# Performance work log

Hardware: AMD Instinct MI355X
Metric: run time of the kernel (lower is better)

The kernel has to match this reference:

```python
import jax, jax.numpy as jnp
import numpy as np

B, S, D, H = 4, 2048, 1024, 16
DK = D // H

def setup_inputs() -> dict:
    key = jax.random.key(0)
    ks = jax.random.split(key, 8)
    query = jax.random.normal(ks[0], (B, S, D), dtype=jnp.float32)
    k_in = jax.random.normal(ks[1], (B, S, D), dtype=jnp.float32)
    v_in = jax.random.normal(ks[2], (B, S, D), dtype=jnp.float32)
    # causal mask: 1 where attending allowed, 0 masked (module masks where mask==0)
    mask = jnp.broadcast_to(jnp.tril(jnp.ones((S, S), dtype=jnp.int32)), (B, S, S))
    s = 1.0 / np.sqrt(D)
    w_q = jax.random.normal(ks[3], (D, D), dtype=jnp.float32) * s
    w_k = jax.random.normal(ks[4], (D, D), dtype=jnp.float32) * s
    w_v = jax.random.normal(ks[5], (D, D), dtype=jnp.float32) * s
    w_o = jax.random.normal(ks[6], (D, D), dtype=jnp.float32) * s
    b_o = jnp.zeros((D,), dtype=jnp.float32)
    return {"query": query, "key": k_in, "value": v_in, "mask": mask,
            "w_q": w_q, "w_k": w_k, "w_v": w_v, "w_o": w_o, "b_o": b_o}

def reference(query, key, value, mask, w_q, w_k, w_v, w_o, b_o):
    b, s, d = query.shape
    # projections (nn.Linear: x @ W.T); weights stored as [out, in]
    Q = (query @ w_q.T).reshape(b, s, H, DK).transpose(0, 2, 1, 3)  # [b,h,s,dk]
    K = (key   @ w_k.T).reshape(b, s, H, DK).transpose(0, 2, 1, 3)
    V = (value @ w_v.T).reshape(b, s, H, DK).transpose(0, 2, 1, 3)
    scores = jnp.einsum('bhqd,bhkd->bhqk', Q, K) / np.sqrt(DK)  # [b,h,s,s]
    m = mask[:, None, :, :]  # broadcast over heads
    scores = jnp.where(m == 0, jnp.float32(-1e9), scores)
    attn = jax.nn.softmax(scores, axis=-1)
    out = jnp.einsum('bhqk,bhkd->bhqd', attn, V)  # [b,h,s,dk]
    out = out.transpose(0, 2, 1, 3).reshape(b, s, d)
    out = out @ w_o.T + b_o
    return (out, attn)
```

## Files before the change

### kernel.cpp

```cpp
#include <hip/hip_runtime.h>
#include <hip/hip_bf16.h>

typedef __attribute__((ext_vector_type(8))) short bf16x8;
typedef __attribute__((ext_vector_type(4))) float f32x4;

constexpr int Bn = 4, Sn = 2048, Dn = 1024, Hn = 16;
constexpr int Mn = Bn * Sn;
constexpr float C_SCALE = 0.18033688f;

static __device__ __forceinline__ unsigned short f2bf(float f) {
  union { float f; unsigned int u; } v; v.f = f;
  unsigned int r = v.u + 0x7fffu + ((v.u >> 16) & 1u);
  return (unsigned short)(r >> 16);
}

static __device__ __forceinline__ unsigned int cvtpk_bf16(float lo, float hi) {
  unsigned int r;
  asm("v_cvt_pk_bf16_f32 %0, %1, %2" : "=v"(r) : "v"(lo), "v"(hi));
  return r;
}

static __device__ __forceinline__ void gload_lds16(const unsigned short* g,
                                                   unsigned short* l) {
  __builtin_amdgcn_global_load_lds(
      (const __attribute__((address_space(1))) unsigned int*)g,
      (__attribute__((address_space(3))) unsigned int*)l,
      16, 0, 0);
}

__global__ __launch_bounds__(256)
void cvt7(const float* __restrict__ q, const float* __restrict__ k,
          const float* __restrict__ v, const float* __restrict__ wq,
          const float* __restrict__ wk, const float* __restrict__ wv,
          const float* __restrict__ wo,
          unsigned short* __restrict__ oq, unsigned short* __restrict__ ok,
          unsigned short* __restrict__ ov, unsigned short* __restrict__ owq,
          unsigned short* __restrict__ owk, unsigned short* __restrict__ owv,
          unsigned short* __restrict__ owo)
{
  constexpr size_t NX = (size_t)Mn * Dn;
  constexpr size_t NW = (size_t)Dn * Dn;
  constexpr size_t total = 3 * NX + 4 * NW;
  size_t e = ((size_t)blockIdx.x * blockDim.x + threadIdx.x) * 4;
  const size_t step = (size_t)gridDim.x * blockDim.x * 4;
  for (; e < total; e += step) {
    int seg; size_t off;
    if (e < 3 * NX) { seg = (int)(e >> 23); off = e & (NX - 1); }
    else { const size_t j = e - 3 * NX; seg = 3 + (int)(j >> 20); off = j & (NW - 1); }
    const float* src; unsigned short* dst;
    switch (seg) {
      case 0: src = q;  dst = oq;  break;
      case 1: src = k;  dst = ok;  break;
      case 2: src = v;  dst = ov;  break;
      case 3: src = wq; dst = owq; break;
      case 4: src = wk; dst = owk; break;
      case 5: src = wv; dst = owv; break;
      default: src = wo; dst = owo; break;
    }
    const float4 val = *(const float4*)(src + off);
    ushort4 o;
    o.x = f2bf(val.x); o.y = f2bf(val.y); o.z = f2bf(val.z); o.w = f2bf(val.w);
    *(ushort4*)(dst + off) = o;
  }
}

static __device__ __forceinline__ void gemm_core(
    const unsigned short* __restrict__ A, const unsigned short* __restrict__ Bw,
    unsigned short* Asl, unsigned short* Bsl,
    int m0, int n0, int wave, int lane, f32x4 (*acc)[4])
{
  const int tid = wave * 64 + lane;
  const int lr = lane & 15, lg = lane >> 4;
  const int wm = wave >> 1, wn = wave & 1;

  for (int k0 = 0; k0 < 1024; k0 += 64) {
    __syncthreads();
    #pragma unroll
    for (int it = 0; it < 4; ++it) {
      const int e = it * 256 + tid;
      const int row = e >> 3;
      const int col = ((e & 7) ^ (row & 7)) * 8;
      gload_lds16(A  + (size_t)(m0 + row) * 1024 + k0 + col,
                  &Asl[(it * 256 + wave * 64) * 8]);
      gload_lds16(Bw + (size_t)(n0 + row) * 1024 + k0 + col,
                  &Bsl[(it * 256 + wave * 64) * 8]);
    }
    __syncthreads();

    #pragma unroll
    for (int kk = 0; kk < 2; ++kk) {
      const int ch = ((kk * 4 + lg) ^ (lr & 7)) * 8;
      bf16x8 af[4], bfr[4];
      #pragma unroll
      for (int mf = 0; mf < 4; ++mf)
        af[mf] = *(const bf16x8*)&Asl[(wm * 64 + mf * 16 + lr) * 64 + ch];
      #pragma unroll
      for (int nf = 0; nf < 4; ++nf)
        bfr[nf] = *(const bf16x8*)&Bsl[(wn * 64 + nf * 16 + lr) * 64 + ch];
      #pragma unroll
      for (int mf = 0; mf < 4; ++mf)
        #pragma unroll
        for (int nf = 0; nf < 4; ++nf)
          acc[mf][nf] = __builtin_amdgcn_mfma_f32_16x16x32_bf16(
              af[mf], bfr[nf], acc[mf][nf], 0, 0, 0);
    }
  }
}

__global__ __launch_bounds__(256)
void gemm_qkv(const unsigned short* __restrict__ Xq,
              const unsigned short* __restrict__ Xk,
              const unsigned short* __restrict__ Xv,
              const unsigned short* __restrict__ Wq,
              const unsigned short* __restrict__ Wk,
              const unsigned short* __restrict__ Wv,
              unsigned short* __restrict__ Qbf,
              unsigned short* __restrict__ Kbf,
              unsigned short* __restrict__ Vtb)
{
  __shared__ unsigned short ShBuf[128 * 136];
  unsigned short* Asl = ShBuf;
  unsigned short* Bsl = ShBuf + 128 * 64;

  const int tid  = threadIdx.x;
  const int wave = tid >> 6, lane = tid & 63;
  const int lr = lane & 15, lg = lane >> 4;
  const int wm = wave >> 1, wn = wave & 1;
  const int m0 = blockIdx.x * 128;
  const int n0 = blockIdx.y * 128;
  const int z  = blockIdx.z;

  const unsigned short* A  = (z == 0) ? Xq : (z == 1) ? Xk : Xv;
  const unsigned short* Bw = (z == 0) ? Wq : (z == 1) ? Wk : Wv;

  f32x4 acc[4][4] = {};
  gemm_core(A, Bw, Asl, Bsl, m0, n0, wave, lane, acc);

  if (z < 2) {
    unsigned short* C = (z == 0) ? Qbf : Kbf;
    const float cs = (z == 0) ? C_SCALE : 1.0f;
    #pragma unroll
    for (int mf = 0; mf < 4; ++mf)
      #pragma unroll
      for (int nf = 0; nf < 4; ++nf)
        #pragma unroll
        for (int i = 0; i < 4; ++i) {
          const int row = m0 + wm * 64 + mf * 16 + lg * 4 + i;
          const int col = n0 + wn * 64 + nf * 16 + lr;
          C[(size_t)row * 1024 + col] = f2bf(acc[mf][nf][i] * cs);
        }
  } else {
    unsigned short (*Ts)[136] = (unsigned short (*)[136])ShBuf;
    __syncthreads();
    #pragma unroll
    for (int mf = 0; mf < 4; ++mf)
      #pragma unroll
      for (int nf = 0; nf < 4; ++nf)
        #pragma unroll
        for (int i = 0; i < 4; ++i)
          Ts[wn * 64 + nf * 16 + lr][wm * 64 + mf * 16 + lg * 4 + i] =
              f2bf(acc[mf][nf][i]);
    __syncthreads();
    const int dkl = tid >> 1;
    const int sh  = (tid & 1) * 64;
    const int b = m0 >> 11, s0 = m0 & 2047;
    const int gcol = n0 + dkl;
    const int h = gcol >> 6, dk = gcol & 63;
    unsigned short* dst =
        Vtb + ((size_t)((b * 16 + h) * 64 + dk)) * Sn + s0 + sh;
    #pragma unroll
    for (int jj = 0; jj < 8; ++jj)
      *(bf16x8*)(dst + jj * 8) = *(const bf16x8*)&Ts[dkl][sh + jj * 8];
  }
}

__global__ __launch_bounds__(256)
void gemm_o(const unsigned short* __restrict__ A,
            const unsigned short* __restrict__ Bw,
            float* __restrict__ C, const float* __restrict__ bias)
{
  __shared__ unsigned short Asl[128 * 64];
  __shared__ unsigned short Bsl[128 * 64];
  const int tid  = threadIdx.x;
  const int wave = tid >> 6, lane = tid & 63;
  const int lr = lane & 15, lg = lane >> 4;
  const int wm = wave >> 1, wn = wave & 1;
  const int m0 = blockIdx.x * 128;
  const int n0 = blockIdx.y * 128;

  f32x4 acc[4][4] = {};
  gemm_core(A, Bw, Asl, Bsl, m0, n0, wave, lane, acc);

  float bv[4];
  #pragma unroll
  for (int nf = 0; nf < 4; ++nf) bv[nf] = bias[n0 + wn * 64 + nf * 16 + lr];
  #pragma unroll
  for (int mf = 0; mf < 4; ++mf)
    #pragma unroll
    for (int nf = 0; nf < 4; ++nf)
      #pragma unroll
      for (int i = 0; i < 4; ++i) {
        const int row = m0 + wm * 64 + mf * 16 + lg * 4 + i;
        const int col = n0 + wn * 64 + nf * 16 + lr;
        C[(size_t)row * 1024 + col] = acc[mf][nf][i] + bv[nf];
      }
}

__global__ __launch_bounds__(128)
void attn_fused(const unsigned short* __restrict__ Qb,
                const unsigned short* __restrict__ Kb,
                const unsigned short* __restrict__ Vt,
                float* __restrict__ attn_out,
                unsigned short* __restrict__ Ob)
{
  __shared__ unsigned short Ps[2][32][88];

  const int tid = threadIdx.x;
  const int w = tid >> 6, lane = tid & 63;
  const int lr = lane & 15, lg = lane >> 4;
  const int wg = (blockIdx.x & 7) * 256 + (blockIdx.x >> 3);
  const int bh = wg >> 5;
  const int j  = wg & 31;
  const int qs = w ? (63 - j) : j;
  const int b = bh >> 4, h = bh & 15;
  const int q0 = qs * 32;
  const int nkt = (q0 + 31) / 64 + 1;
  const int kl  = nkt - 1;

  const unsigned short* Kbh = Kb + (size_t)(b * Sn) * Dn + h * 64;
  const unsigned short* Vbh = Vt + (size_t)(bh * 64) * Sn;
  float* aout = attn_out + (size_t)bh * Sn * (size_t)Sn;

  bf16x8 qf[2][2];
  #pragma unroll
  for (int hf = 0; hf < 2; ++hf) {
    const int qoff = (b * Sn + q0 + hf * 16 + lr) * Dn + h * 64 + lg * 8;
    qf[hf][0] = *(const bf16x8*)(Qb + qoff);
    qf[hf][1] = *(const bf16x8*)(Qb + qoff + 32);
  }

  float l[2] = {0.f, 0.f};

  for (int kt = 0; kt < kl; ++kt) {
    bf16x8 kf[4][2];
    #pragma unroll
    for (int nf = 0; nf < 4; ++nf)
      #pragma unroll
      for (int kk = 0; kk < 2; ++kk)
        kf[nf][kk] = *(const bf16x8*)(
            Kbh + (kt * 64 + nf * 16 + lr) * Dn + kk * 32 + lg * 8);
    __builtin_amdgcn_s_setprio(1);
    #pragma unroll
    for (int hf = 0; hf < 2; ++hf)
      #pragma unroll
      for (int nf = 0; nf < 4; ++nf) {
        f32x4 a = {0.f, 0.f, 0.f, 0.f};
        a = __builtin_amdgcn_mfma_f32_16x16x32_bf16(kf[nf][0], qf[hf][0], a, 0, 0, 0);
        a = __builtin_amdgcn_mfma_f32_16x16x32_bf16(kf[nf][1], qf[hf][1], a, 0, 0, 0);
        l[hf] += (exp2f(a[0]) + exp2f(a[1])) + (exp2f(a[2]) + exp2f(a[3]));
      }
    __builtin_amdgcn_s_setprio(0);
  }
  {
    bf16x8 kf[4][2];
    #pragma unroll
    for (int nf = 0; nf < 4; ++nf)
      #pragma unroll
      for (int kk = 0; kk < 2; ++kk)
        kf[nf][kk] = *(const bf16x8*)(
            Kbh + (kl * 64 + nf * 16 + lr) * Dn + kk * 32 + lg * 8);
    #pragma unroll
    for (int hf = 0; hf < 2; ++hf) {
      const int q = q0 + hf * 16 + lr;
      #pragma unroll
      for (int nf = 0; nf < 4; ++nf) {
        f32x4 a = {0.f, 0.f, 0.f, 0.f};
        a = __builtin_amdgcn_mfma_f32_16x16x32_bf16(kf[nf][0], qf[hf][0], a, 0, 0, 0);
        a = __builtin_amdgcn_mfma_f32_16x16x32_bf16(kf[nf][1], qf[hf][1], a, 0, 0, 0);
        #pragma unroll
        for (int i = 0; i < 4; ++i) {
          const int key = kl * 64 + nf * 16 + lg * 4 + i;
          l[hf] += (key <= q) ? exp2f(a[i]) : 0.f;
        }
      }
    }
  }
  float nlg[2];
  #pragma unroll
  for (int hf = 0; hf < 2; ++hf) {
    l[hf] += __shfl_xor(l[hf], 16, 64);
    l[hf] += __shfl_xor(l[hf], 32, 64);
    nlg[hf] = -log2f(l[hf]);
  }

  f32x4 oacc[2][4] = {};
  for (int kt = 0; kt < nkt; ++kt) {
    const bool last = (kt == kl);
    bf16x8 kf[4][2], vt[4][2];
    #pragma unroll
    for (int nf = 0; nf < 4; ++nf)
      #pragma unroll
      for (int kk = 0; kk < 2; ++kk) {
        kf[nf][kk] = *(const bf16x8*)(
            Kbh + (kt * 64 + nf * 16 + lr) * Dn + kk * 32 + lg * 8);
        vt[nf][kk] = *(const bf16x8*)(
            Vbh + (nf * 16 + lr) * Sn + kt * 64 + kk * 32 + lg * 8);
      }
    #pragma unroll
    for (int hf = 0; hf < 2; ++hf) {
      const int q = q0 + hf * 16 + lr;
      __builtin_amdgcn_s_setprio(1);
      #pragma unroll
      for (int nf = 0; nf < 4; ++nf) {
        f32x4 a = {0.f, 0.f, 0.f, 0.f};
        a = __builtin_amdgcn_mfma_f32_16x16x32_bf16(kf[nf][0], qf[hf][0], a, 0, 0, 0);
        a = __builtin_amdgcn_mfma_f32_16x16x32_bf16(kf[nf][1], qf[hf][1], a, 0, 0, 0);
        f32x4 p4;
        if (!last) {
          #pragma unroll
          for (int i = 0; i < 4; ++i) p4[i] = exp2f(a[i] + nlg[hf]);
        } else {
          #pragma unroll
          for (int i = 0; i < 4; ++i) {
            const int key = kl * 64 + nf * 16 + lg * 4 + i;
            const float v = exp2f(a[i] + nlg[hf]);
            p4[i] = (key <= q) ? v : 0.f;
          }
        }
        __builtin_nontemporal_store(
            p4, (f32x4*)&aout[q * Sn + kt * 64 + nf * 16 + lg * 4]);
        uint2 pk;
        pk.x = cvtpk_bf16(p4[0], p4[1]);
        pk.y = cvtpk_bf16(p4[2], p4[3]);
        *(uint2*)&Ps[w][hf * 16 + lr][nf * 16 + lg * 4] = pk;
      }
      __builtin_amdgcn_s_setprio(0);
    }
    __builtin_amdgcn_s_setprio(1);
    #pragma unroll
    for (int hf = 0; hf < 2; ++hf) {
      bf16x8 pa[2];
      pa[0] = *(const bf16x8*)&Ps[w][hf * 16 + lr][lg * 8];
      pa[1] = *(const bf16x8*)&Ps[w][hf * 16 + lr][32 + lg * 8];
      #pragma unroll
      for (int kk = 0; kk < 2; ++kk)
        #pragma unroll
        for (int nf = 0; nf < 4; ++nf)
          oacc[hf][nf] = __builtin_amdgcn_mfma_f32_16x16x32_bf16(
              pa[kk], vt[nf][kk], oacc[hf][nf], 0, 0, 0);
    }
    __builtin_amdgcn_s_setprio(0);
  }
  for (int kt = nkt; kt < Sn / 64; ++kt) {
    const f32x4 z = {0.f, 0.f, 0.f, 0.f};
    #pragma unroll
    for (int jj = 0; jj < 8; ++jj) {
      const int r = q0 + lg + 4 * jj;
      __builtin_nontemporal_store(
          z, (f32x4*)&aout[r * Sn + kt * 64 + lr * 4]);
    }
  }
  #pragma unroll
  for (int hf = 0; hf < 2; ++hf)
    #pragma unroll
    for (int nf = 0; nf < 4; ++nf)
      #pragma unroll
      for (int i = 0; i < 4; ++i) {
        const int qq = q0 + hf * 16 + lg * 4 + i;
        const int dk = nf * 16 + lr;
        Ob[(b * Sn + qq) * Dn + h * 64 + dk] = f2bf(oacc[hf][nf][i]);
      }
}

extern "C" void kernel_launch(void* const* d_in, const int* in_sizes, int n_in,
                              void* d_out, int out_size, void* d_ws, size_t ws_size,
                              hipStream_t stream)
{
  const float* query = (const float*)d_in[0];
  const float* key   = (const float*)d_in[1];
  const float* value = (const float*)d_in[2];
  const float* w_q = (const float*)d_in[4];
  const float* w_k = (const float*)d_in[5];
  const float* w_v = (const float*)d_in[6];
  const float* w_o = (const float*)d_in[7];
  const float* b_o = (const float*)d_in[8];

  constexpr size_t NX = (size_t)Mn * Dn;
  constexpr size_t NW = (size_t)Dn * Dn;
  unsigned short* Xq  = (unsigned short*)d_ws;
  unsigned short* Xk  = Xq  + NX;
  unsigned short* Xv  = Xk  + NX;
  unsigned short* Wq  = Xv  + NX;
  unsigned short* Wk  = Wq  + NW;
  unsigned short* Wv  = Wk  + NW;
  unsigned short* Wo  = Wv  + NW;
  unsigned short* Qbf = Wo  + NW;
  unsigned short* Kbf = Qbf + NX;
  unsigned short* Vtb = Kbf + NX;
  unsigned short* Obf = Vtb + NX;

  float* out  = (float*)d_out;
  float* attn = out + NX;

  cvt7<<<dim3(2048), dim3(256), 0, stream>>>(query, key, value, w_q, w_k, w_v, w_o,
                                             Xq, Xk, Xv, Wq, Wk, Wv, Wo);
  gemm_qkv<<<dim3(Mn / 128, Dn / 128, 3), dim3(256), 0, stream>>>(
      Xq, Xk, Xv, Wq, Wk, Wv, Qbf, Kbf, Vtb);
  attn_fused<<<dim3(64 * 32), dim3(128), 0, stream>>>(Qbf, Kbf, Vtb, attn, Obf);
  gemm_o<<<dim3(Mn / 128, Dn / 128), dim3(256), 0, stream>>>(Obf, Wo, out, b_o);
}
```

Baseline: 451.9 us.

## Add 256x256 double-buffered 8-wave GEMM for Q/K and output projections

```diff
diff --git a/kernel.cpp b/kernel.cpp
--- a/kernel.cpp
+++ b/kernel.cpp
@@ -64,6 +64,151 @@
   }
 }
 
+#define BARm()  asm volatile("s_barrier" ::: "memory")
+#define LGKM0() do { asm volatile("s_waitcnt lgkmcnt(0)" ::: "memory"); \
+                     __builtin_amdgcn_sched_barrier(0); } while (0)
+#define VM4()   asm volatile("s_waitcnt vmcnt(4)" ::: "memory")
+#define VM0()   asm volatile("s_waitcnt vmcnt(0)" ::: "memory")
+
+static __device__ __forceinline__ bf16x8 ldfrag(const unsigned short* half,
+                                                int row, int colB) {
+  int qb = row * 128 + colB;
+  qb ^= (row & 7) << 4;
+  return *(const bf16x8*)((const char*)half + qb);
+}
+
+#define LA_(d, h) (L + (d) * 32768 + (h) * 8192)
+#define LB_(d, h) (L + (d) * 32768 + 16384 + (h) * 8192)
+#define MYA(d)    (L + (d) * 32768 + wm * 8192)
+#define MYB(d)    (L + (d) * 32768 + 16384 + (wn >> 1) * 8192)
+
+#define STAGE_A(d, h, t) do { \
+  const unsigned short* g_ = Ag + (size_t)(m0 + (h) * 128) * 1024 + (t) * 64; \
+  gload_lds16(g_ + (size_t)sr0 * 1024 + sc0, LA_(d, h) + wid * 512); \
+  gload_lds16(g_ + (size_t)sr1 * 1024 + sc1, LA_(d, h) + 4096 + wid * 512); \
+} while (0)
+
+#define STAGE_B(d, h, t) do { \
+  const unsigned short* g_ = Wg + (size_t)(n0 + (h) * 128) * 1024 + (t) * 64; \
+  gload_lds16(g_ + (size_t)sr0 * 1024 + sc0, LB_(d, h) + wid * 512); \
+  gload_lds16(g_ + (size_t)sr1 * 1024 + sc1, LB_(d, h) + 4096 + wid * 512); \
+} while (0)
+
+#define LDQ0(d) do { \
+  _Pragma("unroll") for (int j = 0; j < 4; ++j) { \
+    Ar[j][0] = ldfrag(MYA(d), j * 16 + lr, lg * 16); \
+    Ar[j][1] = ldfrag(MYA(d), j * 16 + lr, 64 + lg * 16); } \
+  _Pragma("unroll") for (int n = 0; n < 2; ++n) { \
+    Br[n][0] = ldfrag(MYB(d), brow + n * 16 + lr, lg * 16); \
+    Br[n][1] = ldfrag(MYB(d), brow + n * 16 + lr, 64 + lg * 16); } \
+} while (0)
+
+#define LDB23(d) do { \
+  _Pragma("unroll") for (int n = 2; n < 4; ++n) { \
+    Br[n][0] = ldfrag(MYB(d), brow + n * 16 + lr, lg * 16); \
+    Br[n][1] = ldfrag(MYB(d), brow + n * 16 + lr, 64 + lg * 16); } \
+} while (0)
+
+#define LDA47(d) do { \
+  _Pragma("unroll") for (int j = 0; j < 4; ++j) { \
+    Ar[j][0] = ldfrag(MYA(d), 64 + j * 16 + lr, lg * 16); \
+    Ar[j][1] = ldfrag(MYA(d), 64 + j * 16 + lr, 64 + lg * 16); } \
+} while (0)
+
+#define QUAD(mb, nb) do { \
+  __builtin_amdgcn_s_setprio(1); \
+  _Pragma("unroll") for (int j = 0; j < 4; ++j) \
+    _Pragma("unroll") for (int n = 0; n < 2; ++n) \
+      _Pragma("unroll") for (int kk2 = 0; kk2 < 2; ++kk2) \
+        acc[(mb) + j][(nb) + n] = __builtin_amdgcn_mfma_f32_16x16x32_bf16( \
+            Ar[j][kk2], Br[(nb) + n][kk2], acc[(mb) + j][(nb) + n], 0, 0, 0); \
+  __builtin_amdgcn_s_setprio(0); \
+  __builtin_amdgcn_sched_barrier(0); \
+} while (0)
+
+template<int OUT>
+__global__ __launch_bounds__(512)
+void gemm256(const unsigned short* __restrict__ A0,
+             const unsigned short* __restrict__ A1,
+             const unsigned short* __restrict__ W0,
+             const unsigned short* __restrict__ W1,
+             unsigned short* __restrict__ C0,
+             unsigned short* __restrict__ C1,
+             float* __restrict__ Cf, const float* __restrict__ bias)
+{
+  __shared__ __align__(16) unsigned short L[65536];
+  const int tid = threadIdx.x;
+  const int wid = tid >> 6, lane = tid & 63;
+  const int lr = lane & 15, lg = lane >> 4;
+  const int wm = wid >> 2, wn = wid & 3;
+  const int m0 = blockIdx.x * 256;
+  const int n0 = blockIdx.y * 256;
+  const int z  = blockIdx.z;
+  const unsigned short* Ag = z ? A1 : A0;
+  const unsigned short* Wg = z ? W1 : W0;
+  const int brow = (wn & 1) * 64;
+
+  const int sr0 = tid >> 3,          sc0 = ((tid & 7) ^ (sr0 & 7)) * 8;
+  const int sr1 = 64 + (tid >> 3),   sc1 = ((tid & 7) ^ (sr1 & 7)) * 8;
+
+  f32x4 acc[8][4] = {};
+  bf16x8 Ar[4][2], Br[4][2];
+
+  STAGE_A(0, 0, 0); STAGE_A(0, 1, 0);
+  STAGE_B(0, 0, 0); STAGE_B(0, 1, 0);
+  STAGE_B(1, 0, 1); STAGE_B(1, 1, 1);
+  VM4(); BARm();
+
+  for (int i = 0; i < 7; ++i) {
+    const int t1 = 2 * i + 1, t2 = t1 + 1, t3 = t1 + 2;
+    LDQ0(0);  STAGE_A(1, 0, t1); BARm(); LGKM0(); QUAD(0, 0); BARm();
+    LDB23(0); STAGE_A(1, 1, t1); BARm(); LGKM0(); QUAD(0, 2); BARm();
+    LDA47(0); STAGE_B(0, 0, t2); BARm(); LGKM0(); QUAD(4, 2); BARm();
+    STAGE_B(0, 1, t2);           BARm();          QUAD(4, 0); VM4(); BARm();
+    LDQ0(1);  STAGE_A(0, 0, t2); BARm(); LGKM0(); QUAD(0, 0); BARm();
+    LDB23(1); STAGE_A(0, 1, t2); BARm(); LGKM0(); QUAD(0, 2); BARm();
+    LDA47(1); STAGE_B(1, 0, t3); BARm(); LGKM0(); QUAD(4, 2); BARm();
+    STAGE_B(1, 1, t3);           BARm();          QUAD(4, 0); VM4(); BARm();
+  }
+  LDQ0(0);  STAGE_A(1, 0, 15); BARm(); LGKM0(); QUAD(0, 0); BARm();
+  LDB23(0); STAGE_A(1, 1, 15); BARm(); LGKM0(); QUAD(0, 2); BARm();
+  LDA47(0);                    BARm(); LGKM0(); QUAD(4, 2); BARm();
+                               BARm();          QUAD(4, 0); VM0(); BARm();
+  LDQ0(1);                     BARm(); LGKM0(); QUAD(0, 0); BARm();
+  LDB23(1);                    BARm(); LGKM0(); QUAD(0, 2); BARm();
+  LDA47(1);                    BARm(); LGKM0(); QUAD(4, 2); BARm();
+                                                QUAD(4, 0);
+
+  if constexpr (OUT == 0) {
+    unsigned short* C = z ? C1 : C0;
+    const float cs = z ? 1.0f : C_SCALE;
+    #pragma unroll
+    for (int mf = 0; mf < 8; ++mf)
+      #pragma unroll
+      for (int nf = 0; nf < 4; ++nf)
+        #pragma unroll
+        for (int i = 0; i < 4; ++i) {
+          const int row = m0 + wm * 128 + mf * 16 + lg * 4 + i;
+          const int col = n0 + wn * 64 + nf * 16 + lr;
+          C[(size_t)row * 1024 + col] = f2bf(acc[mf][nf][i] * cs);
+        }
+  } else {
+    float bv[4];
+    #pragma unroll
+    for (int nf = 0; nf < 4; ++nf) bv[nf] = bias[n0 + wn * 64 + nf * 16 + lr];
+    #pragma unroll
+    for (int mf = 0; mf < 8; ++mf)
+      #pragma unroll
+      for (int nf = 0; nf < 4; ++nf)
+        #pragma unroll
+        for (int i = 0; i < 4; ++i) {
+          const int row = m0 + wm * 128 + mf * 16 + lg * 4 + i;
+          const int col = n0 + wn * 64 + nf * 16 + lr;
+          Cf[(size_t)row * 1024 + col] = acc[mf][nf][i] + bv[nf];
+        }
+  }
+}
+
 static __device__ __forceinline__ void gemm_core(
     const unsigned short* __restrict__ A, const unsigned short* __restrict__ Bw,
     unsigned short* Asl, unsigned short* Bsl,
@@ -108,15 +253,9 @@
 }
 
 __global__ __launch_bounds__(256)
-void gemm_qkv(const unsigned short* __restrict__ Xq,
-              const unsigned short* __restrict__ Xk,
-              const unsigned short* __restrict__ Xv,
-              const unsigned short* __restrict__ Wq,
-              const unsigned short* __restrict__ Wk,
-              const unsigned short* __restrict__ Wv,
-              unsigned short* __restrict__ Qbf,
-              unsigned short* __restrict__ Kbf,
-              unsigned short* __restrict__ Vtb)
+void gemm_v(const unsigned short* __restrict__ Xv,
+            const unsigned short* __restrict__ Wv,
+            unsigned short* __restrict__ Vtb)
 {
   __shared__ unsigned short ShBuf[128 * 136];
   unsigned short* Asl = ShBuf;
@@ -128,82 +267,31 @@
   const int wm = wave >> 1, wn = wave & 1;
   const int m0 = blockIdx.x * 128;
   const int n0 = blockIdx.y * 128;
-  const int z  = blockIdx.z;
-
-  const unsigned short* A  = (z == 0) ? Xq : (z == 1) ? Xk : Xv;
-  const unsigned short* Bw = (z == 0) ? Wq : (z == 1) ? Wk : Wv;
 
   f32x4 acc[4][4] = {};
-  gemm_core(A, Bw, Asl, Bsl, m0, n0, wave, lane, acc);
-
-  if (z < 2) {
-    unsigned short* C = (z == 0) ? Qbf : Kbf;
-    const float cs = (z == 0) ? C_SCALE : 1.0f;
-    #pragma unroll
-    for (int mf = 0; mf < 4; ++mf)
-      #pragma unroll
-      for (int nf = 0; nf < 4; ++nf)
-        #pragma unroll
-        for (int i = 0; i < 4; ++i) {
-          const int row = m0 + wm * 64 + mf * 16 + lg * 4 + i;
-          const int col = n0 + wn * 64 + nf * 16 + lr;
-          C[(size_t)row * 1024 + col] = f2bf(acc[mf][nf][i] * cs);
-        }
-  } else {
-    unsigned short (*Ts)[136] = (unsigned short (*)[136])ShBuf;
-    __syncthreads();
-    #pragma unroll
-    for (int mf = 0; mf < 4; ++mf)
-      #pragma unroll
-      for (int nf = 0; nf < 4; ++nf)
-        #pragma unroll
-        for (int i = 0; i < 4; ++i)
-          Ts[wn * 64 + nf * 16 + lr][wm * 64 + mf * 16 + lg * 4 + i] =
-              f2bf(acc[mf][nf][i]);
-    __syncthreads();
-    const int dkl = tid >> 1;
-    const int sh  = (tid & 1) * 64;
-    const int b = m0 >> 11, s0 = m0 & 2047;
-    const int gcol = n0 + dkl;
-    const int h = gcol >> 6, dk = gcol & 63;
-    unsigned short* dst =
-        Vtb + ((size_t)((b * 16 + h) * 64 + dk)) * Sn + s0 + sh;
-    #pragma unroll
-    for (int jj = 0; jj < 8; ++jj)
-      *(bf16x8*)(dst + jj * 8) = *(const bf16x8*)&Ts[dkl][sh + jj * 8];
-  }
-}
-
-__global__ __launch_bounds__(256)
-void gemm_o(const unsigned short* __restrict__ A,
-            const unsigned short* __restrict__ Bw,
-            float* __restrict__ C, const float* __restrict__ bias)
-{
-  __shared__ unsigned short Asl[128 * 64];
-  __shared__ unsigned short Bsl[128 * 64];
-  const int tid  = threadIdx.x;
-  const int wave = tid >> 6, lane = tid & 63;
-  const int lr = lane & 15, lg = lane >> 4;
-  const int wm = wave >> 1, wn = wave & 1;
-  const int m0 = blockIdx.x * 128;
-  const int n0 = blockIdx.y * 128;
-
-  f32x4 acc[4][4] = {};
-  gemm_core(A, Bw, Asl, Bsl, m0, n0, wave, lane, acc);
-
-  float bv[4];
-  #pragma unroll
-  for (int nf = 0; nf < 4; ++nf) bv[nf] = bias[n0 + wn * 64 + nf * 16 + lr];
+  gemm_core(Xv, Wv, Asl, Bsl, m0, n0, wave, lane, acc);
+
+  unsigned short (*Ts)[136] = (unsigned short (*)[136])ShBuf;
+  __syncthreads();
   #pragma unroll
   for (int mf = 0; mf < 4; ++mf)
     #pragma unroll
     for (int nf = 0; nf < 4; ++nf)
       #pragma unroll
-      for (int i = 0; i < 4; ++i) {
-        const int row = m0 + wm * 64 + mf * 16 + lg * 4 + i;
-        const int col = n0 + wn * 64 + nf * 16 + lr;
-        C[(size_t)row * 1024 + col] = acc[mf][nf][i] + bv[nf];
-      }
+      for (int i = 0; i < 4; ++i)
+        Ts[wn * 64 + nf * 16 + lr][wm * 64 + mf * 16 + lg * 4 + i] =
+            f2bf(acc[mf][nf][i]);
+  __syncthreads();
+  const int dkl = tid >> 1;
+  const int sh  = (tid & 1) * 64;
+  const int b = m0 >> 11, s0 = m0 & 2047;
+  const int gcol = n0 + dkl;
+  const int h = gcol >> 6, dk = gcol & 63;
+  unsigned short* dst =
+      Vtb + ((size_t)((b * 16 + h) * 64 + dk)) * Sn + s0 + sh;
+  #pragma unroll
+  for (int jj = 0; jj < 8; ++jj)
+    *(bf16x8*)(dst + jj * 8) = *(const bf16x8*)&Ts[dkl][sh + jj * 8];
 }
 
 __global__ __launch_bounds__(128)
@@ -404,8 +492,10 @@
 
   cvt7<<<dim3(2048), dim3(256), 0, stream>>>(query, key, value, w_q, w_k, w_v, w_o,
                                              Xq, Xk, Xv, Wq, Wk, Wv, Wo);
-  gemm_qkv<<<dim3(Mn / 128, Dn / 128, 3), dim3(256), 0, stream>>>(
-      Xq, Xk, Xv, Wq, Wk, Wv, Qbf, Kbf, Vtb);
+  gemm256<0><<<dim3(Mn / 256, Dn / 256, 2), dim3(512), 0, stream>>>(
+      Xq, Xk, Wq, Wk, Qbf, Kbf, nullptr, nullptr);
+  gemm_v<<<dim3(Mn / 128, Dn / 128), dim3(256), 0, stream>>>(Xv, Wv, Vtb);
   attn_fused<<<dim3(64 * 32), dim3(128), 0, stream>>>(Qbf, Kbf, Vtb, attn, Obf);
-  gemm_o<<<dim3(Mn / 128, Dn / 128), dim3(256), 0, stream>>>(Obf, Wo, out, b_o);
-}
+  gemm256<1><<<dim3(Mn / 256, Dn / 256, 1), dim3(512), 0, stream>>>(
+      Obf, nullptr, Wo, nullptr, nullptr, nullptr, out, b_o);
+}
```

Measured after the change: 458.4 us. Within noise of the previous version (+1.4%).
